# Kernel optimization log

Hardware: AMD Instinct MI355X
Metric: run time of the kernel (lower is better)

## Reference

```python
import jax, jax.numpy as jnp
import numpy as np

EPS = 0.1  # FAConv default eps

def setup_inputs() -> dict:
    N, E, D, OUT = 100000, 640000, 128, 128
    key = jax.random.key(0)
    k = jax.random.split(key, 8)
    x = jax.random.normal(k[0], (N, D), dtype=jnp.float32)
    x_0 = jax.random.normal(k[1], (N, D), dtype=jnp.float32)
    edge_index = jax.random.randint(k[2], (2, E), 0, N, dtype=jnp.int64)
    edge_weight = jax.random.uniform(k[3], (E,), dtype=jnp.float32)
    # FAConv attention vectors: Linear(D, 1, bias=False) each
    att_l = jax.random.normal(k[4], (D,), dtype=jnp.float32) / np.sqrt(D)
    att_r = jax.random.normal(k[5], (D,), dtype=jnp.float32) / np.sqrt(D)
    # trailing Linear(D, OUT)
    W = jax.random.normal(k[6], (OUT, D), dtype=jnp.float32) / np.sqrt(D)
    b = jax.random.normal(k[7], (OUT,), dtype=jnp.float32) * 0.01
    return {"x": x, "x_0": x_0, "edge_weight": edge_weight,
            "att_l": att_l, "att_r": att_r, "W": W, "b": b,
            "edge_index": edge_index}

def reference(x, x_0, edge_weight, att_l, att_r, W, b, edge_index):
    N = x.shape[0]
    src, dst = edge_index[0], edge_index[1]  # messages flow src(j) -> dst(i)
    # per-node attention logits (cheap GEMV), then per-edge gather
    alpha_l = x @ att_l  # [N] for source side (att_l -> _j)
    alpha_r = x @ att_r  # [N] for target side (att_r -> _i)
    alpha = jnp.tanh(alpha_l[src] + alpha_r[dst])  # [E]
    coeff = alpha * edge_weight                    # [E]
    msg = coeff[:, None] * x[src]                  # [E, D] gather + scale
    agg = jax.ops.segment_sum(msg, dst, num_segments=N)  # scatter-add [N, D]
    out = EPS * x_0 + agg
    out = jax.nn.relu(out)
    return out @ W.T + b
```

## Files before the change

### kernel.cpp

```cpp
#include <hip/hip_runtime.h>

#define DD 128
#define EPSV 0.1f
#define CAP 32

typedef __attribute__((ext_vector_type(8))) short bf16x8;
typedef __attribute__((ext_vector_type(4))) float f32x4;

static __device__ __forceinline__ unsigned bf16rne(float f) {
    unsigned u = __float_as_uint(f);
    return (u + 0x7fffu + ((u >> 16) & 1u)) >> 16;
}

__global__ __launch_bounds__(256) void k_alpha(const float* __restrict__ x,
        const float* __restrict__ attl, const float* __restrict__ attr,
        float* __restrict__ al, float* __restrict__ ar,
        unsigned* __restrict__ xbf, int N)
{
    int gid  = blockIdx.x * 256 + threadIdx.x;
    int node = gid >> 6;
    int lane = threadIdx.x & 63;
    if (node >= N) return;
    float2 xv = *reinterpret_cast<const float2*>(x + (size_t)node * DD + lane * 2);
    xbf[(size_t)node * 64 + lane] = (bf16rne(xv.y) << 16) | bf16rne(xv.x);
    float2 lv = *reinterpret_cast<const float2*>(attl + lane * 2);
    float2 rv = *reinterpret_cast<const float2*>(attr + lane * 2);
    float pl = xv.x * lv.x + xv.y * lv.y;
    float pr = xv.x * rv.x + xv.y * rv.y;
#pragma unroll
    for (int off = 32; off > 0; off >>= 1) {
        pl += __shfl_xor(pl, off, 64);
        pr += __shfl_xor(pr, off, 64);
    }
    if (lane == 0) { al[node] = pl; ar[node] = pr; }
}

__global__ __launch_bounds__(256) void k_fill(const int* __restrict__ ei,
        const float* __restrict__ ew, const float* __restrict__ al,
        const float* __restrict__ ar, int* __restrict__ cnt,
        int2* __restrict__ bkt, int E)
{
    int e = blockIdx.x * 256 + threadIdx.x;
    if (e >= E) return;
    int s = ei[e];
    int d = ei[E + e];
    float c = tanhf(al[s] + ar[d]) * ew[e];
    int pos = atomicAdd(&cnt[d], 1);
    if (pos < CAP) bkt[(size_t)d * CAP + pos] = make_int2(s, __float_as_int(c));
}

__global__ __launch_bounds__(256) void k_agg(const unsigned* __restrict__ xbf,
        const float* __restrict__ xz, const int* __restrict__ cnt,
        const int2* __restrict__ bkt, unsigned* __restrict__ hbf, int N)
{
    int gid  = blockIdx.x * 256 + threadIdx.x;
    int node = gid >> 6;
    int lane = threadIdx.x & 63;
    if (node >= N) return;
    int deg = cnt[node];
    if (deg > CAP) deg = CAP;
    const int2* pp = bkt + (size_t)node * CAP;
    float accx = 0.f, accy = 0.f;
    for (int j = 0; j < deg; j += 8) {
        int  src[8];
        float cf[8];
#pragma unroll
        for (int i = 0; i < 8; ++i) {
            int2 q = pp[j + i];
            bool act = (j + i) < deg;
            src[i] = act ? q.x : 0;
            cf[i]  = act ? __int_as_float(q.y) : 0.f;
        }
        unsigned u[8];
#pragma unroll
        for (int i = 0; i < 8; ++i)
            u[i] = xbf[(size_t)src[i] * 64 + lane];
#pragma unroll
        for (int i = 0; i < 8; ++i) {
            accx += cf[i] * __uint_as_float(u[i] << 16);
            accy += cf[i] * __uint_as_float(u[i] & 0xFFFF0000u);
        }
    }
    float2 z = *reinterpret_cast<const float2*>(xz + (size_t)node * DD + lane * 2);
    float ox = fmaxf(EPSV * z.x + accx, 0.f);
    float oy = fmaxf(EPSV * z.y + accy, 0.f);
    hbf[(size_t)node * 64 + lane] = (bf16rne(oy) << 16) | bf16rne(ox);
}

__global__ __launch_bounds__(256) void k_wb(const float* __restrict__ W,
        unsigned* __restrict__ WB)
{
    int i = blockIdx.x * 256 + threadIdx.x;
    int g    = i & 3;
    int lane = (i >> 2) & 63;
    int kk   = (i >> 8) & 3;
    int tile = i >> 10;
    int col = tile * 16 + (lane & 15);
    int k   = kk * 32 + (lane >> 4) * 8 + g * 2;
    unsigned lo = bf16rne(W[col * DD + k]);
    unsigned hi = bf16rne(W[col * DD + k + 1]);
    WB[i] = (hi << 16) | lo;
}

__global__ __launch_bounds__(256) void k_out(const unsigned* __restrict__ hbf,
        const unsigned* __restrict__ WB, const float* __restrict__ bias,
        float* __restrict__ out, int N)
{
    int wv = threadIdx.x >> 6;
    int l  = threadIdx.x & 63;
    int rowBase = blockIdx.x * 64 + wv * 16;
    if (rowBase >= N) return;
    int arow = rowBase + (l & 15);
    int lrow = arow < N ? arow : N - 1;
    int g = l >> 4;

    f32x4 acc[8];
#pragma unroll
    for (int t = 0; t < 8; ++t) acc[t] = (f32x4){0.f, 0.f, 0.f, 0.f};

    const uint4* ha = reinterpret_cast<const uint4*>(hbf + (size_t)lrow * 64);
    const uint4* wb = reinterpret_cast<const uint4*>(WB);
#pragma unroll
    for (int kk = 0; kk < 4; ++kk) {
        uint4 av = ha[kk * 4 + g];
        bf16x8 a = *reinterpret_cast<bf16x8*>(&av);
#pragma unroll
        for (int t = 0; t < 8; ++t) {
            uint4 bv = wb[(t * 4 + kk) * 64 + l];
            bf16x8 b = *reinterpret_cast<bf16x8*>(&bv);
            acc[t] = __builtin_amdgcn_mfma_f32_16x16x32_bf16(a, b, acc[t], 0, 0, 0);
        }
    }

#pragma unroll
    for (int t = 0; t < 8; ++t) {
        int col = t * 16 + (l & 15);
        float bv = bias[col];
#pragma unroll
        for (int r = 0; r < 4; ++r) {
            int row = rowBase + g * 4 + r;
            if (row < N)
                out[(size_t)row * DD + col] = acc[t][r] + bv;
        }
    }
}

extern "C" void kernel_launch(void* const* d_in, const int* in_sizes, int n_in,
                              void* d_out, int out_size, void* d_ws, size_t ws_size,
                              hipStream_t stream) {
    const float* x    = (const float*)d_in[0];
    const float* xz   = (const float*)d_in[1];
    const float* ew   = (const float*)d_in[2];
    const float* attl = (const float*)d_in[3];
    const float* attr = (const float*)d_in[4];
    const float* W    = (const float*)d_in[5];
    const float* bias = (const float*)d_in[6];
    const int*   ei   = (const int*)d_in[7];
    float* out = (float*)d_out;

    int N = in_sizes[0] / DD;
    int E = in_sizes[2];

    float*    al  = (float*)d_ws;
    float*    ar  = al + N;
    int*      cnt = (int*)(ar + N);
    int2*     bkt = (int2*)(cnt + N);
    unsigned* WB  = (unsigned*)(bkt + (size_t)N * CAP);
    unsigned* xbf = WB + 8192;
    unsigned* hbf = xbf + (size_t)N * 64;

    hipMemsetAsync(cnt, 0, (size_t)N * sizeof(int), stream);
    k_alpha<<<(N + 3) / 4, 256, 0, stream>>>(x, attl, attr, al, ar, xbf, N);
    k_wb   <<<32, 256, 0, stream>>>(W, WB);
    k_fill <<<(E + 255) / 256, 256, 0, stream>>>(ei, ew, al, ar, cnt, bkt, E);
    k_agg  <<<(N + 3) / 4, 256, 0, stream>>>(xbf, xz, cnt, bkt, hbf, N);
    k_out  <<<(N + 63) / 64, 256, 0, stream>>>(hbf, WB, bias, out, N);
}
```

Measured before the change: 273.3 us.

## Aggregate with 16 lanes per node and 16-byte gathers, zero-fill bucket slots

The aggregation kernel now maps 16 lanes to each node, and each lane gathers 16 bytes (8 bf16 features) per neighbour instead of 4 bytes. The first 8 bucket slots are loaded unconditionally, which relies on a new prep kernel that zeroes slots 0-7 of every bucket. That prep kernel also replaces the memset and the W-conversion kernel, so there are fewer launches. In exchange it adds a write pass over part of the bucket array and raises register pressure in the aggregation kernel.

```diff
diff --git a/kernel.cpp b/kernel.cpp
--- a/kernel.cpp
+++ b/kernel.cpp
@@ -10,6 +10,30 @@
 static __device__ __forceinline__ unsigned bf16rne(float f) {
     unsigned u = __float_as_uint(f);
     return (u + 0x7fffu + ((u >> 16) & 1u)) >> 16;
+}
+
+__global__ __launch_bounds__(256) void k_prep(const float* __restrict__ W,
+        unsigned* __restrict__ WB, int* __restrict__ cnt,
+        int4* __restrict__ bkt4, int N)
+{
+    int i = blockIdx.x * 256 + threadIdx.x;
+    if (i < 8192) {
+        int g    = i & 3;
+        int lane = (i >> 2) & 63;
+        int kk   = (i >> 8) & 3;
+        int tile = i >> 10;
+        int col = tile * 16 + (lane & 15);
+        int k   = kk * 32 + (lane >> 4) * 8 + g * 2;
+        unsigned lo = bf16rne(W[col * DD + k]);
+        unsigned hi = bf16rne(W[col * DD + k + 1]);
+        WB[i] = (hi << 16) | lo;
+    }
+    if (i < N) cnt[i] = 0;
+    if (i < N * 4) {
+        int node = i >> 2;
+        int slot = i & 3;
+        bkt4[node * (CAP / 2) + slot] = make_int4(0, 0, 0, 0);
+    }
 }
 
 __global__ __launch_bounds__(256) void k_alpha(const float* __restrict__ x,
@@ -54,52 +78,74 @@
         const int2* __restrict__ bkt, unsigned* __restrict__ hbf, int N)
 {
     int gid  = blockIdx.x * 256 + threadIdx.x;
-    int node = gid >> 6;
-    int lane = threadIdx.x & 63;
+    int l    = threadIdx.x & 63;
+    int li   = l & 15;
+    int node = (gid >> 6) * 4 + (l >> 4);
     if (node >= N) return;
+
+    const int2* pp = bkt + (size_t)node * CAP;
     int deg = cnt[node];
     if (deg > CAP) deg = CAP;
-    const int2* pp = bkt + (size_t)node * CAP;
-    float accx = 0.f, accy = 0.f;
-    for (int j = 0; j < deg; j += 8) {
-        int  src[8];
-        float cf[8];
+
+    const uint4* xr = reinterpret_cast<const uint4*>(xbf);
+    float acc[8];
+#pragma unroll
+    for (int i = 0; i < 8; ++i) acc[i] = 0.f;
+
+    int2 q[8];
+#pragma unroll
+    for (int i = 0; i < 8; ++i) q[i] = pp[i];
+    uint4 u[8];
+#pragma unroll
+    for (int i = 0; i < 8; ++i) u[i] = xr[(size_t)q[i].x * 16 + li];
+#pragma unroll
+    for (int i = 0; i < 8; ++i) {
+        float c = __int_as_float(q[i].y);
+        acc[0] += c * __uint_as_float(u[i].x << 16);
+        acc[1] += c * __uint_as_float(u[i].x & 0xFFFF0000u);
+        acc[2] += c * __uint_as_float(u[i].y << 16);
+        acc[3] += c * __uint_as_float(u[i].y & 0xFFFF0000u);
+        acc[4] += c * __uint_as_float(u[i].z << 16);
+        acc[5] += c * __uint_as_float(u[i].z & 0xFFFF0000u);
+        acc[6] += c * __uint_as_float(u[i].w << 16);
+        acc[7] += c * __uint_as_float(u[i].w & 0xFFFF0000u);
+    }
+
+    for (int j = 8; j < deg; j += 8) {
 #pragma unroll
         for (int i = 0; i < 8; ++i) {
-            int2 q = pp[j + i];
+            int2 qq = pp[j + i];
             bool act = (j + i) < deg;
-            src[i] = act ? q.x : 0;
-            cf[i]  = act ? __int_as_float(q.y) : 0.f;
+            int s   = act ? qq.x : 0;
+            float c = act ? __int_as_float(qq.y) : 0.f;
+            uint4 uu = xr[(size_t)s * 16 + li];
+            acc[0] += c * __uint_as_float(uu.x << 16);
+            acc[1] += c * __uint_as_float(uu.x & 0xFFFF0000u);
+            acc[2] += c * __uint_as_float(uu.y << 16);
+            acc[3] += c * __uint_as_float(uu.y & 0xFFFF0000u);
+            acc[4] += c * __uint_as_float(uu.z << 16);
+            acc[5] += c * __uint_as_float(uu.z & 0xFFFF0000u);
+            acc[6] += c * __uint_as_float(uu.w << 16);
+            acc[7] += c * __uint_as_float(uu.w & 0xFFFF0000u);
         }
-        unsigned u[8];
-#pragma unroll
-        for (int i = 0; i < 8; ++i)
-            u[i] = xbf[(size_t)src[i] * 64 + lane];
-#pragma unroll
-        for (int i = 0; i < 8; ++i) {
-            accx += cf[i] * __uint_as_float(u[i] << 16);
-            accy += cf[i] * __uint_as_float(u[i] & 0xFFFF0000u);
-        }
-    }
-    float2 z = *reinterpret_cast<const float2*>(xz + (size_t)node * DD + lane * 2);
-    float ox = fmaxf(EPSV * z.x + accx, 0.f);
-    float oy = fmaxf(EPSV * z.y + accy, 0.f);
-    hbf[(size_t)node * 64 + lane] = (bf16rne(oy) << 16) | bf16rne(ox);
-}
-
-__global__ __launch_bounds__(256) void k_wb(const float* __restrict__ W,
-        unsigned* __restrict__ WB)
-{
-    int i = blockIdx.x * 256 + threadIdx.x;
-    int g    = i & 3;
-    int lane = (i >> 2) & 63;
-    int kk   = (i >> 8) & 3;
-    int tile = i >> 10;
-    int col = tile * 16 + (lane & 15);
-    int k   = kk * 32 + (lane >> 4) * 8 + g * 2;
-    unsigned lo = bf16rne(W[col * DD + k]);
-    unsigned hi = bf16rne(W[col * DD + k + 1]);
-    WB[i] = (hi << 16) | lo;
+    }
+
+    const float4* zr = reinterpret_cast<const float4*>(xz + (size_t)node * DD + li * 8);
+    float4 z0 = zr[0], z1 = zr[1];
+    float o0 = fmaxf(EPSV * z0.x + acc[0], 0.f);
+    float o1 = fmaxf(EPSV * z0.y + acc[1], 0.f);
+    float o2 = fmaxf(EPSV * z0.z + acc[2], 0.f);
+    float o3 = fmaxf(EPSV * z0.w + acc[3], 0.f);
+    float o4 = fmaxf(EPSV * z1.x + acc[4], 0.f);
+    float o5 = fmaxf(EPSV * z1.y + acc[5], 0.f);
+    float o6 = fmaxf(EPSV * z1.z + acc[6], 0.f);
+    float o7 = fmaxf(EPSV * z1.w + acc[7], 0.f);
+    uint4 w;
+    w.x = (bf16rne(o1) << 16) | bf16rne(o0);
+    w.y = (bf16rne(o3) << 16) | bf16rne(o2);
+    w.z = (bf16rne(o5) << 16) | bf16rne(o4);
+    w.w = (bf16rne(o7) << 16) | bf16rne(o6);
+    reinterpret_cast<uint4*>(hbf)[(size_t)node * 16 + li] = w;
 }
 
 __global__ __launch_bounds__(256) void k_out(const unsigned* __restrict__ hbf,
@@ -169,10 +215,10 @@
     unsigned* xbf = WB + 8192;
     unsigned* hbf = xbf + (size_t)N * 64;
 
-    hipMemsetAsync(cnt, 0, (size_t)N * sizeof(int), stream);
+    int prepThreads = N * 4;
+    k_prep <<<(prepThreads + 255) / 256, 256, 0, stream>>>(W, WB, cnt, (int4*)bkt, N);
     k_alpha<<<(N + 3) / 4, 256, 0, stream>>>(x, attl, attr, al, ar, xbf, N);
-    k_wb   <<<32, 256, 0, stream>>>(W, WB);
     k_fill <<<(E + 255) / 256, 256, 0, stream>>>(ei, ew, al, ar, cnt, bkt, E);
-    k_agg  <<<(N + 3) / 4, 256, 0, stream>>>(xbf, xz, cnt, bkt, hbf, N);
+    k_agg  <<<(N + 15) / 16, 256, 0, stream>>>(xbf, xz, cnt, bkt, hbf, N);
     k_out  <<<(N + 63) / 64, 256, 0, stream>>>(hbf, WB, bias, out, N);
 }
```

Result: faster. 260.4 us (-4.7%).
